# Kernel tuning notes

Measured on AMD Instinct MI355X. Metric: run time of the kernel, lower is better.

Reference implementation:

```python
import jax, jax.numpy as jnp
import numpy as np

# ---- DiTAC constants (from init_kwargs) ----
NC = 10          # tess (number of cells on [0,1])
A_LO = -0.5      # a: lower edge of active range
B_HI = 2.0       # b: upper edge of active range
INV_SQRT2 = 0.7071067811865476


def make_basis(nc):
    """Null-space basis B ([2*nc, nc-1]) of the CPA constraint matrix
    (velocity continuity at internal knots + zero boundary), via QR
    of L^T with mode='complete' ('qr' basis in difw).
    Per-cell velocity v_c(x) = a_c*x + b_c, Avees layout [a0,b0,a1,b1,...]."""
    L = np.zeros((nc + 1, 2 * nc))
    for i in range(1, nc):                      # continuity at x_i = i/nc
        xi = i / nc
        L[i - 1, 2 * (i - 1)] = xi
        L[i - 1, 2 * (i - 1) + 1] = 1.0
        L[i - 1, 2 * i] = -xi
        L[i - 1, 2 * i + 1] = -1.0
    L[nc - 1, 1] = 1.0                          # v(0) = 0  ->  b_0 = 0
    L[nc, 2 * (nc - 1)] = 1.0                   # v(1) = 0  ->  a_{nc-1}+b_{nc-1}=0
    L[nc, 2 * (nc - 1) + 1] = 1.0
    q, _ = np.linalg.qr(L.T, mode='complete')
    return q[:, nc + 1:]                        # [2*nc, nc-1]

_B_NP = make_basis(NC)


def cpab_transform(xn, A, nc):
    """Closed-form integration of the piecewise-affine ODE dx/dt = a_c x + b_c
    for t=1, vectorized over all elements. Fixed nc+1 iterations: each
    iteration either finishes (flow stays inside current cell) or advances
    the point to the next cell boundary and deducts the transit time.
    Once finished, t=0 makes psi == x, a stable fixed point."""
    h = 1.0 / nc
    eps = 1e-12
    c = jnp.clip(jnp.floor(xn * nc).astype(jnp.int32), 0, nc - 1)
    t = jnp.ones_like(xn)
    x = xn
    for _ in range(nc + 1):
        a = A[c, 0]
        b = A[c, 1]
        v = a * x + b
        big_a = jnp.abs(a) > 1e-8
        a_safe = jnp.where(big_a, a, 1.0)
        ea = jnp.exp(t * a)
        psi = jnp.where(big_a, ea * x + (b / a_safe) * (ea - 1.0), x + t * b)
        left = c.astype(x.dtype) * h
        right = left + h
        inside = (psi >= left) & (psi <= right)
        xb = jnp.where(v >= 0, right, left)          # boundary being approached
        vb = a * xb + b
        v_safe = jnp.where(jnp.abs(v) > eps, v, jnp.where(v >= 0, eps, -eps))
        t_aff = jnp.log(jnp.maximum(vb / v_safe, eps)) / a_safe
        b_safe = jnp.where(jnp.abs(b) > eps, b, eps)
        t_hit = jnp.where(big_a, t_aff, (xb - x) / b_safe)
        x = jnp.where(inside, psi, xb)
        t = jnp.where(inside, 0.0, jnp.maximum(t - t_hit, 0.0))
        step = jnp.where(v >= 0, 1, -1)
        c = jnp.where(inside, c, jnp.clip(c + step, 0, nc - 1))
    return x


def setup_inputs() -> dict:
    key = jax.random.key(0)
    k1, k2 = jax.random.split(key)
    x = jax.random.normal(k1, (4096, 2048), dtype=jnp.float32)
    thetas = jax.random.normal(k2, (1, NC - 1), dtype=jnp.float32)
    return {"x": x, "thetas": thetas}


def reference(x, thetas):
    B = jnp.asarray(_B_NP, dtype=x.dtype)                 # [2*nc, nc-1]
    A = (B @ thetas[0]).reshape(NC, 2)                    # per-cell (a, b)
    flat = x.reshape(-1)
    mask = (flat >= A_LO) & (flat <= B_HI)
    masked = jnp.where(mask, flat, 0.0)
    xn = (masked - A_LO) / (B_HI - A_LO)                  # norm to [0,1]
    xt = cpab_transform(xn, A, NC)
    data_t = xt * (B_HI - A_LO) + A_LO                    # denorm to [a,b]
    cpab_out = jnp.where(mask, data_t, flat)
    phi = 0.5 * (1.0 + jax.lax.erf(flat * INV_SQRT2))     # Gaussian CDF gate
    return (cpab_out * phi).reshape(x.shape)
```

## Files before the change

kernel.cpp:

```cpp
#include <hip/hip_runtime.h>
#include <math.h>
#include <string.h>

#define NCELLS 10
#define A_LO  -0.5f
#define B_HI   2.0f

#define TBL_LO    -6.5f
#define TBL_HI     6.5f
#define TBL_SCALE  256.0f
#define TBL_BIAS   1664.0f
#define TBL_N      3329
#define TBL_N_PAD  3332

struct BMat { float v[2 * NCELLS][NCELLS - 1]; };

static void compute_B_host(BMat* out) {
    const int m = 2 * NCELLS;
    const int n = NCELLS + 1;
    double A[2 * NCELLS][NCELLS + 1];
    memset(A, 0, sizeof(A));
    for (int i = 1; i < NCELLS; ++i) {
        double xi = (double)i / NCELLS;
        A[2 * (i - 1)][i - 1]     = xi;
        A[2 * (i - 1) + 1][i - 1] = 1.0;
        A[2 * i][i - 1]           = -xi;
        A[2 * i + 1][i - 1]       = -1.0;
    }
    A[1][NCELLS - 1] = 1.0;
    A[2 * (NCELLS - 1)][NCELLS] = 1.0;
    A[2 * (NCELLS - 1) + 1][NCELLS] = 1.0;

    double V[NCELLS + 1][2 * NCELLS];
    double tau[NCELLS + 1];
    for (int j = 0; j < n; ++j) {
        double alpha = A[j][j];
        double xnorm2 = 0.0;
        for (int i = j + 1; i < m; ++i) xnorm2 += A[i][j] * A[i][j];
        for (int i = 0; i < m; ++i) V[j][i] = 0.0;
        V[j][j] = 1.0;
        if (xnorm2 == 0.0) { tau[j] = 0.0; continue; }
        double beta = -copysign(sqrt(alpha * alpha + xnorm2), alpha);
        tau[j] = (beta - alpha) / beta;
        double scale = 1.0 / (alpha - beta);
        for (int i = j + 1; i < m; ++i) V[j][i] = A[i][j] * scale;
        A[j][j] = beta;
        for (int i = j + 1; i < m; ++i) A[i][j] = 0.0;
        for (int k = j + 1; k < n; ++k) {
            double dot = 0.0;
            for (int i = j; i < m; ++i) dot += V[j][i] * A[i][k];
            dot *= tau[j];
            for (int i = j; i < m; ++i) A[i][k] -= V[j][i] * dot;
        }
    }
    for (int c = 0; c < NCELLS - 1; ++c) {
        double q[2 * NCELLS];
        for (int i = 0; i < m; ++i) q[i] = 0.0;
        q[n + c] = 1.0;
        for (int j = n - 1; j >= 0; --j) {
            double dot = 0.0;
            for (int i = j; i < m; ++i) dot += V[j][i] * q[i];
            dot *= tau[j];
            for (int i = j; i < m; ++i) q[i] -= V[j][i] * dot;
        }
        for (int i = 0; i < m; ++i) out->v[i][c] = (float)q[i];
    }
}

__global__ __launch_bounds__(256) void ditac_prep(
        const float* __restrict__ theta, float* __restrict__ tbl, BMat B) {
    __shared__ float As[2 * NCELLS];
    if (threadIdx.x < 2 * NCELLS) {
        float s = 0.f;
        #pragma unroll
        for (int k = 0; k < NCELLS - 1; ++k) s += B.v[threadIdx.x][k] * theta[k];
        As[threadIdx.x] = s;
    }
    __syncthreads();

    int j = blockIdx.x * blockDim.x + threadIdx.x;
    if (j >= TBL_N_PAD) return;
    if (j >= TBL_N) { tbl[j] = 0.f; return; }

    float f = TBL_LO + (float)j * (1.0f / TBL_SCALE);
    bool mask = (f >= A_LO) && (f <= B_HI);
    float cpab_out = f;
    if (mask) {
        float xn = (f - A_LO) * 0.4f;
        float xx = xn;
        int c = min(max((int)floorf(xn * (float)NCELLS), 0), NCELLS - 1);
        float t = 1.0f;
        #pragma unroll 1
        for (int it = 0; it < NCELLS + 1; ++it) {
            float a = As[2 * c];
            float b = As[2 * c + 1];
            float v = fmaf(a, xx, b);
            bool big_a = fabsf(a) > 1e-8f;
            float a_safe = big_a ? a : 1.0f;
            float ea = __expf(t * a);
            float psi = big_a ? fmaf(ea, xx, (b / a_safe) * (ea - 1.0f))
                              : fmaf(t, b, xx);
            float left  = (float)c * 0.1f;
            float right = left + 0.1f;
            bool inside = (psi >= left) && (psi <= right);
            if (inside) { xx = psi; break; }
            float xb = (v >= 0.f) ? right : left;
            float vb = fmaf(a, xb, b);
            float t_hit;
            if (big_a) {
                float v_safe = (fabsf(v) > 1e-12f) ? v : ((v >= 0.f) ? 1e-12f : -1e-12f);
                t_hit = __logf(fmaxf(vb / v_safe, 1e-12f)) / a_safe;
            } else {
                float b_safe = (fabsf(b) > 1e-12f) ? b : 1e-12f;
                t_hit = (xb - xx) / b_safe;
            }
            xx = xb;
            t = fmaxf(t - t_hit, 0.f);
            c = min(max(c + ((v >= 0.f) ? 1 : -1), 0), NCELLS - 1);
        }
        cpab_out = fmaf(xx, 2.5f, A_LO);
    }
    float phi = 0.5f * (1.0f + erff(f * 0.7071067811865476f));
    tbl[j] = cpab_out * phi;
}

__global__ __launch_bounds__(256) void ditac_main(
        const float4* __restrict__ x, float4* __restrict__ out,
        const float* __restrict__ tbl) {
    __shared__ float T[TBL_N_PAD];
    const int tid = threadIdx.x;
    const int base = blockIdx.x * 2048 + tid;

    float4 vv[8];
    #pragma unroll
    for (int k = 0; k < 8; ++k) vv[k] = x[base + k * 256];

    const float4* t4 = reinterpret_cast<const float4*>(tbl);
    float4* T4 = reinterpret_cast<float4*>(T);
    #pragma unroll
    for (int j = 0; j < TBL_N_PAD / 4; j += 256)
        if (j + tid < TBL_N_PAD / 4) T4[j + tid] = t4[j + tid];
    __syncthreads();

    #pragma unroll
    for (int k = 0; k < 8; ++k) {
        float in[4] = {vv[k].x, vv[k].y, vv[k].z, vv[k].w};
        float r[4];
        #pragma unroll
        for (int e = 0; e < 4; ++e) {
            float f = in[e];
            float u = fmaf(f, TBL_SCALE, TBL_BIAS);
            float uc = fminf(fmaxf(u, 0.0f), (float)(TBL_N - 1));
            int i = min((int)uc, TBL_N - 2);
            float frac = uc - (float)i;
            float lo = T[i];
            float hi = T[i + 1];
            float val = fmaf(frac, hi - lo, lo);
            r[e] = (f > TBL_HI) ? f : val;
        }
        out[base + k * 256] = make_float4(r[0], r[1], r[2], r[3]);
    }
}

extern "C" void kernel_launch(void* const* d_in, const int* in_sizes, int n_in,
                              void* d_out, int out_size, void* d_ws, size_t ws_size,
                              hipStream_t stream) {
    const float* x     = (const float*)d_in[0];
    const float* theta = (const float*)d_in[1];
    float* out = (float*)d_out;
    float* tbl = (float*)d_ws;

    BMat B;
    compute_B_host(&B);

    ditac_prep<<<(TBL_N_PAD + 255) / 256, 256, 0, stream>>>(theta, tbl, B);

    ditac_main<<<1024, 256, 0, stream>>>(
        (const float4*)x, (float4*)out, tbl);
}
```

Baseline: 22.58 us.

## Fuse table construction into main kernel, recomputing the lookup table per block

Removes the separate prep kernel and the global workspace table. Each block now computes the per-cell affine coefficients and then evaluates all lookup table nodes directly into shared memory before interpolating its elements. This drops a kernel launch and the global-to-shared table copy. In exchange every block repeats the full table evaluation, adding redundant transcendental work ahead of the stores.

```diff
diff --git a/kernel.cpp b/kernel.cpp
--- a/kernel.cpp
+++ b/kernel.cpp
@@ -67,22 +67,7 @@
     }
 }
 
-__global__ __launch_bounds__(256) void ditac_prep(
-        const float* __restrict__ theta, float* __restrict__ tbl, BMat B) {
-    __shared__ float As[2 * NCELLS];
-    if (threadIdx.x < 2 * NCELLS) {
-        float s = 0.f;
-        #pragma unroll
-        for (int k = 0; k < NCELLS - 1; ++k) s += B.v[threadIdx.x][k] * theta[k];
-        As[threadIdx.x] = s;
-    }
-    __syncthreads();
-
-    int j = blockIdx.x * blockDim.x + threadIdx.x;
-    if (j >= TBL_N_PAD) return;
-    if (j >= TBL_N) { tbl[j] = 0.f; return; }
-
-    float f = TBL_LO + (float)j * (1.0f / TBL_SCALE);
+__device__ __forceinline__ float eval_node(float f, const float* As) {
     bool mask = (f >= A_LO) && (f <= B_HI);
     float cpab_out = f;
     if (mask) {
@@ -121,12 +106,13 @@
         cpab_out = fmaf(xx, 2.5f, A_LO);
     }
     float phi = 0.5f * (1.0f + erff(f * 0.7071067811865476f));
-    tbl[j] = cpab_out * phi;
+    return cpab_out * phi;
 }
 
-__global__ __launch_bounds__(256) void ditac_main(
+__global__ __launch_bounds__(256) void ditac_fused(
         const float4* __restrict__ x, float4* __restrict__ out,
-        const float* __restrict__ tbl) {
+        const float* __restrict__ theta, BMat B) {
+    __shared__ float As[2 * NCELLS];
     __shared__ float T[TBL_N_PAD];
     const int tid = threadIdx.x;
     const int base = blockIdx.x * 2048 + tid;
@@ -135,11 +121,19 @@
     #pragma unroll
     for (int k = 0; k < 8; ++k) vv[k] = x[base + k * 256];
 
-    const float4* t4 = reinterpret_cast<const float4*>(tbl);
-    float4* T4 = reinterpret_cast<float4*>(T);
-    #pragma unroll
-    for (int j = 0; j < TBL_N_PAD / 4; j += 256)
-        if (j + tid < TBL_N_PAD / 4) T4[j + tid] = t4[j + tid];
+    if (tid < 2 * NCELLS) {
+        float s = 0.f;
+        #pragma unroll
+        for (int k = 0; k < NCELLS - 1; ++k) s += B.v[tid][k] * theta[k];
+        As[tid] = s;
+    }
+    __syncthreads();
+
+    #pragma unroll 1
+    for (int j = tid; j < TBL_N; j += 256) {
+        float f = TBL_LO + (float)j * (1.0f / TBL_SCALE);
+        T[j] = eval_node(f, As);
+    }
     __syncthreads();
 
     #pragma unroll
@@ -168,13 +162,10 @@
     const float* x     = (const float*)d_in[0];
     const float* theta = (const float*)d_in[1];
     float* out = (float*)d_out;
-    float* tbl = (float*)d_ws;
 
     BMat B;
     compute_B_host(&B);
 
-    ditac_prep<<<(TBL_N_PAD + 255) / 256, 256, 0, stream>>>(theta, tbl, B);
-
-    ditac_main<<<1024, 256, 0, stream>>>(
-        (const float4*)x, (float4*)out, tbl);
+    ditac_fused<<<1024, 256, 0, stream>>>(
+        (const float4*)x, (float4*)out, theta, B);
 }
```

Measured after the change: 22.13 us. -2.0%, faster.
